# Kernel tuning notes

Measured on AMD Instinct MI355X. Metric: run time of the kernel, lower is better.

The kernel has to match this reference:

```python
import jax, jax.numpy as jnp
import numpy as np

B, L, F, H, DIM = 32, 1024, 1024, 1024, 1024


def setup_inputs() -> dict:
    key = jax.random.key(0)
    ks = jax.random.split(key, 8)
    features = jax.random.normal(ks[0], (B, L, F), dtype=jnp.float32)
    hidden = jax.random.normal(ks[1], (B, H), dtype=jnp.float32)
    # Dense layer params (glorot-ish scale)
    W1 = jax.random.normal(ks[2], (F, DIM), dtype=jnp.float32) / np.sqrt(F)
    b1 = jnp.zeros((DIM,), dtype=jnp.float32)
    W2 = jax.random.normal(ks[3], (H, DIM), dtype=jnp.float32) / np.sqrt(H)
    b2 = jnp.zeros((DIM,), dtype=jnp.float32)
    Wp = jax.random.normal(ks[4], (DIM, 1), dtype=jnp.float32) / np.sqrt(DIM)
    bp = jnp.zeros((1,), dtype=jnp.float32)
    return {"features": features, "hidden": hidden, "W1": W1, "b1": b1,
            "W2": W2, "b2": b2, "Wp": Wp, "bp": bp}


def reference(features, hidden, W1, b1, W2, b2, Wp, bp):
    # features: [B, L, F], hidden: [B, H]
    h1 = jnp.einsum('blf,fd->bld', features, W1) + b1          # [B, L, D]
    h2 = (hidden @ W2 + b2)[:, None, :]                         # [B, 1, D]
    att = jnp.tanh(h1 + h2)                                     # [B, L, D]
    score = jnp.einsum('bld,do->blo', att, Wp) + bp             # [B, L, 1]
    attention_weights = jax.nn.softmax(score, axis=1)           # [B, L, 1]
    context_vector = jnp.sum(attention_weights * features, axis=1)  # [B, F]
    return context_vector
```

## Files before the change

kernel.cpp:

```cpp
#include <hip/hip_runtime.h>
#include <hip/hip_bf16.h>


typedef __attribute__((ext_vector_type(8))) __bf16 bf16x8;
typedef __attribute__((ext_vector_type(4))) float f32x4;

static __device__ __forceinline__ ushort f2bf(float x) {
  unsigned u = __float_as_uint(x);
  return (ushort)((u + 0x7fffu + ((u >> 16) & 1u)) >> 16);
}

static __device__ __forceinline__ bf16x8 cvt8(float4 lo, float4 hi) {
  __hip_bfloat162 c0 = __float22bfloat162_rn({lo.x, lo.y});
  __hip_bfloat162 c1 = __float22bfloat162_rn({lo.z, lo.w});
  __hip_bfloat162 c2 = __float22bfloat162_rn({hi.x, hi.y});
  __hip_bfloat162 c3 = __float22bfloat162_rn({hi.z, hi.w});
  union { int4 i; bf16x8 v; } u;
  u.i.x = *(int*)&c0; u.i.y = *(int*)&c1; u.i.z = *(int*)&c2; u.i.w = *(int*)&c3;
  return u.v;
}

static __device__ __forceinline__ float tanh_fast(float x) {
  float e = __expf(2.f * x);
  return 1.f - 2.f / (e + 1.f);
}

__global__ __launch_bounds__(256) void prep_kernel(
    const float* __restrict__ W1, ushort* __restrict__ w1t,
    const float* __restrict__ hidden, const float* __restrict__ W2,
    const float* __restrict__ b2, float* __restrict__ h2p) {
  __shared__ float smem[64 * 65];
  const int bx = blockIdx.x, tid = threadIdx.x;
  if (bx < 256) {
    const int tc = bx & 15, tr = bx >> 4;
    float (*tt)[65] = (float(*)[65])smem;
    const int r = tid >> 4, c4 = (tid & 15) * 4;
#pragma unroll
    for (int p = 0; p < 4; ++p) {
      const int rr = p * 16 + r;
      float4 v = *(const float4*)(W1 + (size_t)(tr * 64 + rr) * 1024 + tc * 64 + c4);
      tt[rr][c4] = v.x; tt[rr][c4 + 1] = v.y; tt[rr][c4 + 2] = v.z; tt[rr][c4 + 3] = v.w;
    }
    __syncthreads();
    const int cc = tid >> 3, r8 = (tid & 7) * 8;
#pragma unroll
    for (int p = 0; p < 2; ++p) {
      const int c = p * 32 + cc;
      ushort tmp[8];
#pragma unroll
      for (int j = 0; j < 8; ++j) tmp[j] = f2bf(tt[r8 + j][c]);
      *(int4*)(w1t + (size_t)(tc * 64 + c) * 1024 + tr * 64 + r8) = *(int4*)tmp;
    }
  } else {
    const int t = bx - 256;
    const int dblk = t & 3, b = (t >> 2) & 31, z = t >> 7;
    const int d = dblk * 256 + tid;
    const int k0 = z * 128;
    float* h = smem;
    if (tid < 128) h[tid] = hidden[b * 1024 + k0 + tid];
    __syncthreads();
    float acc = (z == 0) ? b2[d] : 0.f;
#pragma unroll 8
    for (int k = 0; k < 128; ++k)
      acc += h[k] * W2[(size_t)(k0 + k) * 1024 + d];
    h2p[z * 32768 + b * 1024 + d] = acc;
  }
}


#define MFMA_ROW(AF, I)                                                        \
  acc[I][0] = __builtin_amdgcn_mfma_f32_16x16x32_bf16(AF, bf0, acc[I][0], 0, 0, 0); \
  acc[I][1] = __builtin_amdgcn_mfma_f32_16x16x32_bf16(AF, bf1, acc[I][1], 0, 0, 0); \
  acc[I][2] = __builtin_amdgcn_mfma_f32_16x16x32_bf16(AF, bf2, acc[I][2], 0, 0, 0); \
  acc[I][3] = __builtin_amdgcn_mfma_f32_16x16x32_bf16(AF, bf3, acc[I][3], 0, 0, 0);

#define TILE_STEP(T, CUR, NXT, AVIN, AVOUT) {                                  \
                                                      \
    bf16x8 bf0 = *(const bf16x8*)(bb + (T) * 32);                              \
    bf16x8 bf1 = *(const bf16x8*)(bb + 16384 + (T) * 32);                      \
    bf16x8 bf2 = *(const bf16x8*)(bb + 32768 + (T) * 32);                      \
    bf16x8 bf3 = *(const bf16x8*)(bb + 49152 + (T) * 32);                      \
                                                     \
    if ((T) + 2 < 32) {                                                        \
      const float* ap_ = feat + (size_t)(row0 + ar) * 1024 + ((T) + 2) * 32 + akof; \
      AVOUT[0] = *(const float4*)(ap_);                                        \
      AVOUT[1] = *(const float4*)(ap_ + 4);                                    \
      AVOUT[2] = *(const float4*)(ap_ + 8);                                    \
      AVOUT[3] = *(const float4*)(ap_ + 12);                                   \
    }                                                                          \
                                                    \
    bf16x8 af0 = *(const bf16x8*)&ldsA[CUR][wm * 64 + lrow][cswz8];            \
    bf16x8 af1 = *(const bf16x8*)&ldsA[CUR][wm * 64 + 16 + lrow][cswz8];       \
    bf16x8 af2 = *(const bf16x8*)&ldsA[CUR][wm * 64 + 32 + lrow][cswz8];       \
    bf16x8 af3 = *(const bf16x8*)&ldsA[CUR][wm * 64 + 48 + lrow][cswz8];       \
    MFMA_ROW(af0, 0); MFMA_ROW(af1, 1); MFMA_ROW(af2, 2); MFMA_ROW(af3, 3);    \
                                     \
    if ((T) + 1 < 32) {                                                        \
      union { bf16x8 v; int4 i; } w0_, w1_;                                    \
      w0_.v = cvt8(AVIN[0], AVIN[1]);                                          \
      w1_.v = cvt8(AVIN[2], AVIN[3]);                                          \
      *(int4*)&ldsA[NXT][ar][awz0] = w0_.i;                                    \
      *(int4*)&ldsA[NXT][ar][awz1] = w1_.i;                                    \
    }                                                                          \
    __syncthreads();                                                           \
  }

__global__ __launch_bounds__(256, 3) void gemm_score_kernel(
    const float* __restrict__ feat,
    const ushort* __restrict__ w1t,
    const float* __restrict__ b1, const float* __restrict__ h2p,
    const float* __restrict__ wp, float* __restrict__ score_p) {
  __shared__ ushort ldsA[2][128][32];
  __shared__ float sred[2][64];
  __shared__ float hbl[128], wpl[128];

  const int tid = threadIdx.x;
  const int row0 = blockIdx.x * 128;
  const int col0 = blockIdx.y * 128;
  const int b = blockIdx.x >> 3;

  const int wave = tid >> 6, lane = tid & 63;
  const int wm = wave & 1, wn = wave >> 1;
  const int lrow = lane & 15, quad = lane >> 4;
  const int cswz8 = (quad ^ ((lrow >> 1) & 3)) * 8;

  if (tid < 128) {
    const int d = col0 + tid;
    float hv = b1[d];
#pragma unroll
    for (int p = 0; p < 8; ++p) hv += h2p[p * 32768 + b * 1024 + d];
    hbl[tid] = hv;
  } else {
    wpl[tid - 128] = wp[col0 + tid - 128];
  }

  const int ar = tid >> 1;
  const int akof = (tid & 1) * 16;
  const int xr = (ar >> 1) & 3;
  const int awz0 = ((2 * (tid & 1) + 0) ^ xr) * 8;
  const int awz1 = ((2 * (tid & 1) + 1) ^ xr) * 8;

  const ushort* bb = w1t + (size_t)(col0 + wn * 64 + lrow) * 1024 + quad * 8;

  f32x4 acc[4][4] = {};
  float4 avA[4], avB[4];

  {
    const float* ap_ = feat + (size_t)(row0 + ar) * 1024 + akof;
    float4 v0 = *(const float4*)(ap_);
    float4 v1 = *(const float4*)(ap_ + 4);
    float4 v2 = *(const float4*)(ap_ + 8);
    float4 v3 = *(const float4*)(ap_ + 12);
    union { bf16x8 v; int4 i; } w0_, w1_;
    w0_.v = cvt8(v0, v1);
    w1_.v = cvt8(v2, v3);
    *(int4*)&ldsA[0][ar][awz0] = w0_.i;
    *(int4*)&ldsA[0][ar][awz1] = w1_.i;
    const float* ap1_ = ap_ + 32;
    avA[0] = *(const float4*)(ap1_);
    avA[1] = *(const float4*)(ap1_ + 4);
    avA[2] = *(const float4*)(ap1_ + 8);
    avA[3] = *(const float4*)(ap1_ + 12);
  }
  __syncthreads();

  for (int t = 0; t < 32; t += 2) {
    TILE_STEP(t, 0, 1, avA, avB);
    TILE_STEP(t + 1, 1, 0, avB, avA);
  }

  float hbv[4], wpv[4];
#pragma unroll
  for (int j = 0; j < 4; ++j) {
    const int idx = wn * 64 + j * 16 + lrow;
    hbv[j] = hbl[idx];
    wpv[j] = wpl[idx];
  }
  float rsum[4][4];
#pragma unroll
  for (int i = 0; i < 4; ++i) {
#pragma unroll
    for (int r = 0; r < 4; ++r) {
      float s = 0.f;
#pragma unroll
      for (int j = 0; j < 4; ++j)
        s += tanh_fast(acc[i][j][r] + hbv[j]) * wpv[j];
      s += __shfl_xor(s, 8);
      s += __shfl_xor(s, 4);
      s += __shfl_xor(s, 2);
      s += __shfl_xor(s, 1);
      rsum[i][r] = s;
    }
  }
  if (wn == 1 && lrow == 0) {
#pragma unroll
    for (int i = 0; i < 4; ++i)
#pragma unroll
      for (int r = 0; r < 4; ++r)
        sred[wm][i * 16 + quad * 4 + r] = rsum[i][r];
  }
  __syncthreads();
  if (wn == 0 && lrow == 0) {
#pragma unroll
    for (int i = 0; i < 4; ++i)
#pragma unroll
      for (int r = 0; r < 4; ++r) {
        const int ro = wm * 64 + i * 16 + quad * 4 + r;
        score_p[(size_t)blockIdx.y * 32768 + row0 + ro] =
            rsum[i][r] + sred[wm][ro & 63];
      }
  }
}

__global__ __launch_bounds__(256) void softmax_kernel(
    const float* __restrict__ score_p, float* __restrict__ w,
    float* __restrict__ out) {
  const int b = blockIdx.x, tid = threadIdx.x;
  const int lane = tid & 63, wv = tid >> 6;
  __shared__ float sm[4], ss[4];
  float v[4];
  float mx = -1e30f;
#pragma unroll
  for (int i = 0; i < 4; ++i) {
    const int idx = b * 1024 + i * 256 + tid;
    out[idx] = 0.f;
    float s = 0.f;
#pragma unroll
    for (int p = 0; p < 8; ++p) s += score_p[p * 32768 + idx];
    v[i] = s;
    mx = fmaxf(mx, s);
  }
#pragma unroll
  for (int off = 32; off; off >>= 1) mx = fmaxf(mx, __shfl_xor(mx, off));
  if (lane == 0) sm[wv] = mx;
  __syncthreads();
  mx = fmaxf(fmaxf(sm[0], sm[1]), fmaxf(sm[2], sm[3]));
  float sum = 0.f;
#pragma unroll
  for (int i = 0; i < 4; ++i) {
    v[i] = __expf(v[i] - mx);
    sum += v[i];
  }
#pragma unroll
  for (int off = 32; off; off >>= 1) sum += __shfl_xor(sum, off);
  if (lane == 0) ss[wv] = sum;
  __syncthreads();
  const float inv = 1.f / (ss[0] + ss[1] + ss[2] + ss[3]);
#pragma unroll
  for (int i = 0; i < 4; ++i) w[b * 1024 + i * 256 + tid] = v[i] * inv;
}

__global__ __launch_bounds__(256) void context_kernel(
    const float* __restrict__ w, const float* __restrict__ feat,
    float* __restrict__ out) {
  const int b = blockIdx.y;
  const int l0 = blockIdx.x * 64;
  const int f0 = threadIdx.x * 4;
  __shared__ float wl[64];
  if (threadIdx.x < 64) wl[threadIdx.x] = w[b * 1024 + l0 + threadIdx.x];
  __syncthreads();
  const float* fb = feat + (size_t)b * 1048576 + (size_t)l0 * 1024 + f0;
  float a0 = 0.f, a1 = 0.f, a2 = 0.f, a3 = 0.f;
#pragma unroll 8
  for (int l = 0; l < 64; ++l) {
    float4 v = *(const float4*)(fb + (size_t)l * 1024);
    const float wv = wl[l];
    a0 += wv * v.x;
    a1 += wv * v.y;
    a2 += wv * v.z;
    a3 += wv * v.w;
  }
  float* dst = out + b * 1024 + f0;
  atomicAdd(dst + 0, a0);
  atomicAdd(dst + 1, a1);
  atomicAdd(dst + 2, a2);
  atomicAdd(dst + 3, a3);
}

extern "C" void kernel_launch(void* const* d_in, const int* in_sizes, int n_in,
                              void* d_out, int out_size, void* d_ws, size_t ws_size,
                              hipStream_t stream) {
  const float* feat   = (const float*)d_in[0];
  const float* hidden = (const float*)d_in[1];
  const float* W1     = (const float*)d_in[2];
  const float* b1     = (const float*)d_in[3];
  const float* W2     = (const float*)d_in[4];
  const float* b2     = (const float*)d_in[5];
  const float* Wp     = (const float*)d_in[6];
  float* out = (float*)d_out;

  char* ws = (char*)d_ws;
  ushort* w1t    = (ushort*)ws;
  float* score_p = (float*)(ws + 2097152);
  float* h2p     = (float*)(ws + 3145728);
  float* wts     = (float*)(ws + 4194304);

  prep_kernel<<<1280, 256, 0, stream>>>(W1, w1t, hidden, W2, b2, h2p);
  gemm_score_kernel<<<dim3(256, 8), 256, 0, stream>>>(feat, w1t, b1, h2p, Wp,
                                                      score_p);
  softmax_kernel<<<32, 256, 0, stream>>>(score_p, wts, out);
  context_kernel<<<dim3(16, 32), 256, 0, stream>>>(wts, feat, out);
}
```

Before: 398.0 us.

## Make each GEMM block cover all columns so features are read once

The score GEMM is reorganised so each 512-thread block owns 64 rows and the full 1024 output columns, eight waves with 128 columns each. The fp32 features are then read and converted to bf16 only once instead of eight times across column blocks, and the partial-score buffer plus its reduction in softmax go away. B fragments are double-buffered in registers, with manual barriers and setprio around the MFMA burst. In exchange the tile is larger, which raises register pressure, the grid is smaller, and W1 is streamed by every block.

```diff
diff --git a/kernel.cpp b/kernel.cpp
--- a/kernel.cpp
+++ b/kernel.cpp
@@ -10,14 +10,13 @@
   return (ushort)((u + 0x7fffu + ((u >> 16) & 1u)) >> 16);
 }
 
-static __device__ __forceinline__ bf16x8 cvt8(float4 lo, float4 hi) {
-  __hip_bfloat162 c0 = __float22bfloat162_rn({lo.x, lo.y});
-  __hip_bfloat162 c1 = __float22bfloat162_rn({lo.z, lo.w});
-  __hip_bfloat162 c2 = __float22bfloat162_rn({hi.x, hi.y});
-  __hip_bfloat162 c3 = __float22bfloat162_rn({hi.z, hi.w});
-  union { int4 i; bf16x8 v; } u;
-  u.i.x = *(int*)&c0; u.i.y = *(int*)&c1; u.i.z = *(int*)&c2; u.i.w = *(int*)&c3;
-  return u.v;
+static __device__ __forceinline__ int2 cvt4(float4 v) {
+  __hip_bfloat162 c0 = __float22bfloat162_rn({v.x, v.y});
+  __hip_bfloat162 c1 = __float22bfloat162_rn({v.z, v.w});
+  int2 r;
+  r.x = *(int*)&c0;
+  r.y = *(int*)&c1;
+  return r;
 }
 
 static __device__ __forceinline__ float tanh_fast(float x) {
@@ -68,113 +67,99 @@
 }
 
 
-#define MFMA_ROW(AF, I)                                                        \
-  acc[I][0] = __builtin_amdgcn_mfma_f32_16x16x32_bf16(AF, bf0, acc[I][0], 0, 0, 0); \
-  acc[I][1] = __builtin_amdgcn_mfma_f32_16x16x32_bf16(AF, bf1, acc[I][1], 0, 0, 0); \
-  acc[I][2] = __builtin_amdgcn_mfma_f32_16x16x32_bf16(AF, bf2, acc[I][2], 0, 0, 0); \
-  acc[I][3] = __builtin_amdgcn_mfma_f32_16x16x32_bf16(AF, bf3, acc[I][3], 0, 0, 0);
-
-#define TILE_STEP(T, CUR, NXT, AVIN, AVOUT) {                                  \
-                                                      \
-    bf16x8 bf0 = *(const bf16x8*)(bb + (T) * 32);                              \
-    bf16x8 bf1 = *(const bf16x8*)(bb + 16384 + (T) * 32);                      \
-    bf16x8 bf2 = *(const bf16x8*)(bb + 32768 + (T) * 32);                      \
-    bf16x8 bf3 = *(const bf16x8*)(bb + 49152 + (T) * 32);                      \
-                                                     \
-    if ((T) + 2 < 32) {                                                        \
-      const float* ap_ = feat + (size_t)(row0 + ar) * 1024 + ((T) + 2) * 32 + akof; \
-      AVOUT[0] = *(const float4*)(ap_);                                        \
-      AVOUT[1] = *(const float4*)(ap_ + 4);                                    \
-      AVOUT[2] = *(const float4*)(ap_ + 8);                                    \
-      AVOUT[3] = *(const float4*)(ap_ + 12);                                   \
-    }                                                                          \
-                                                    \
-    bf16x8 af0 = *(const bf16x8*)&ldsA[CUR][wm * 64 + lrow][cswz8];            \
-    bf16x8 af1 = *(const bf16x8*)&ldsA[CUR][wm * 64 + 16 + lrow][cswz8];       \
-    bf16x8 af2 = *(const bf16x8*)&ldsA[CUR][wm * 64 + 32 + lrow][cswz8];       \
-    bf16x8 af3 = *(const bf16x8*)&ldsA[CUR][wm * 64 + 48 + lrow][cswz8];       \
-    MFMA_ROW(af0, 0); MFMA_ROW(af1, 1); MFMA_ROW(af2, 2); MFMA_ROW(af3, 3);    \
-                                     \
-    if ((T) + 1 < 32) {                                                        \
-      union { bf16x8 v; int4 i; } w0_, w1_;                                    \
-      w0_.v = cvt8(AVIN[0], AVIN[1]);                                          \
-      w1_.v = cvt8(AVIN[2], AVIN[3]);                                          \
-      *(int4*)&ldsA[NXT][ar][awz0] = w0_.i;                                    \
-      *(int4*)&ldsA[NXT][ar][awz1] = w1_.i;                                    \
-    }                                                                          \
-    __syncthreads();                                                           \
-  }
-
-__global__ __launch_bounds__(256, 3) void gemm_score_kernel(
+__global__ __launch_bounds__(512, 2) void gemm_score_kernel(
     const float* __restrict__ feat,
     const ushort* __restrict__ w1t,
     const float* __restrict__ b1, const float* __restrict__ h2p,
-    const float* __restrict__ wp, float* __restrict__ score_p) {
-  __shared__ ushort ldsA[2][128][32];
-  __shared__ float sred[2][64];
-  __shared__ float hbl[128], wpl[128];
+    const float* __restrict__ wp, float* __restrict__ score) {
+  __shared__ ushort ldsA[2][64][32];
+  __shared__ float hbl[1024], wpl[1024];
+  __shared__ float sred[7][64];
 
   const int tid = threadIdx.x;
-  const int row0 = blockIdx.x * 128;
-  const int col0 = blockIdx.y * 128;
-  const int b = blockIdx.x >> 3;
-
+  const int row0 = blockIdx.x * 64;
+  const int b = blockIdx.x >> 4;
   const int wave = tid >> 6, lane = tid & 63;
-  const int wm = wave & 1, wn = wave >> 1;
   const int lrow = lane & 15, quad = lane >> 4;
-  const int cswz8 = (quad ^ ((lrow >> 1) & 3)) * 8;
-
-  if (tid < 128) {
-    const int d = col0 + tid;
-    float hv = b1[d];
-#pragma unroll
-    for (int p = 0; p < 8; ++p) hv += h2p[p * 32768 + b * 1024 + d];
-    hbl[tid] = hv;
-  } else {
-    wpl[tid - 128] = wp[col0 + tid - 128];
-  }
-
-  const int ar = tid >> 1;
-  const int akof = (tid & 1) * 16;
-  const int xr = (ar >> 1) & 3;
-  const int awz0 = ((2 * (tid & 1) + 0) ^ xr) * 8;
-  const int awz1 = ((2 * (tid & 1) + 1) ^ xr) * 8;
-
-  const ushort* bb = w1t + (size_t)(col0 + wn * 64 + lrow) * 1024 + quad * 8;
-
-  f32x4 acc[4][4] = {};
-  float4 avA[4], avB[4];
 
   {
-    const float* ap_ = feat + (size_t)(row0 + ar) * 1024 + akof;
-    float4 v0 = *(const float4*)(ap_);
-    float4 v1 = *(const float4*)(ap_ + 4);
-    float4 v2 = *(const float4*)(ap_ + 8);
-    float4 v3 = *(const float4*)(ap_ + 12);
-    union { bf16x8 v; int4 i; } w0_, w1_;
-    w0_.v = cvt8(v0, v1);
-    w1_.v = cvt8(v2, v3);
-    *(int4*)&ldsA[0][ar][awz0] = w0_.i;
-    *(int4*)&ldsA[0][ar][awz1] = w1_.i;
-    const float* ap1_ = ap_ + 32;
-    avA[0] = *(const float4*)(ap1_);
-    avA[1] = *(const float4*)(ap1_ + 4);
-    avA[2] = *(const float4*)(ap1_ + 8);
-    avA[3] = *(const float4*)(ap1_ + 12);
-  }
-  __syncthreads();
-
-  for (int t = 0; t < 32; t += 2) {
-    TILE_STEP(t, 0, 1, avA, avB);
-    TILE_STEP(t + 1, 1, 0, avB, avA);
-  }
-
-  float hbv[4], wpv[4];
-#pragma unroll
-  for (int j = 0; j < 4; ++j) {
-    const int idx = wn * 64 + j * 16 + lrow;
-    hbv[j] = hbl[idx];
-    wpv[j] = wpl[idx];
+    const int d = tid * 2;
+    float2 hv = *(const float2*)(b1 + d);
+#pragma unroll
+    for (int p = 0; p < 8; ++p) {
+      float2 hp = *(const float2*)(h2p + p * 32768 + b * 1024 + d);
+      hv.x += hp.x;
+      hv.y += hp.y;
+    }
+    *(float2*)(hbl + d) = hv;
+    *(float2*)(wpl + d) = *(const float2*)(wp + d);
+  }
+
+  const int ar = tid >> 3;
+  const int asw = ((((tid & 7) >> 1) ^ ((ar >> 1) & 3)) * 8 + (tid & 1) * 4);
+  const float* aptr = feat + (size_t)(row0 + ar) * 1024 + (tid & 7) * 4;
+
+  const int acs = (quad ^ ((lrow >> 1) & 3)) * 8;
+
+  const ushort* bb[8];
+#pragma unroll
+  for (int j = 0; j < 8; ++j)
+    bb[j] = w1t + (size_t)(wave * 128 + j * 16 + lrow) * 1024 + quad * 8;
+
+  f32x4 acc[4][8] = {};
+  float4 avv[2];
+  bf16x8 bB[2][8];
+
+  {
+    float4 v0 = *(const float4*)(aptr);
+    *(int2*)&ldsA[0][ar][asw] = cvt4(v0);
+    avv[1] = *(const float4*)(aptr + 32);
+    avv[0] = *(const float4*)(aptr + 64);
+#pragma unroll
+    for (int j = 0; j < 8; ++j) bB[0][j] = *(const bf16x8*)(bb[j]);
+  }
+  asm volatile("s_waitcnt lgkmcnt(0)");
+  __builtin_amdgcn_sched_barrier(0);
+  __builtin_amdgcn_s_barrier();
+  __builtin_amdgcn_sched_barrier(0);
+
+#pragma unroll
+  for (int t = 0; t < 32; ++t) {
+    const int cur = t & 1, nxt = cur ^ 1;
+    bf16x8 af[4];
+#pragma unroll
+    for (int i = 0; i < 4; ++i)
+      af[i] = *(const bf16x8*)&ldsA[cur][i * 16 + lrow][acs];
+    if (t + 1 < 32) {
+#pragma unroll
+      for (int j = 0; j < 8; ++j)
+        bB[nxt][j] = *(const bf16x8*)(bb[j] + (t + 1) * 32);
+    }
+    if (t + 1 < 32)
+      *(int2*)&ldsA[nxt][ar][asw] = cvt4(avv[(t + 1) & 1]);
+    if (t + 3 < 32)
+      avv[(t + 1) & 1] = *(const float4*)(aptr + (t + 3) * 32);
+    __builtin_amdgcn_s_setprio(1);
+#pragma unroll
+    for (int i = 0; i < 4; ++i)
+#pragma unroll
+      for (int j = 0; j < 8; ++j)
+        acc[i][j] = __builtin_amdgcn_mfma_f32_16x16x32_bf16(
+            af[i], bB[cur][j], acc[i][j], 0, 0, 0);
+    __builtin_amdgcn_s_setprio(0);
+    __builtin_amdgcn_sched_barrier(0);
+    asm volatile("s_waitcnt lgkmcnt(0)");
+    __builtin_amdgcn_sched_barrier(0);
+    __builtin_amdgcn_s_barrier();
+    __builtin_amdgcn_sched_barrier(0);
+  }
+
+  float hbv[8], wpv[8];
+#pragma unroll
+  for (int j = 0; j < 8; ++j) {
+    const int c = wave * 128 + j * 16 + lrow;
+    hbv[j] = hbl[c];
+    wpv[j] = wpl[c];
   }
   float rsum[4][4];
 #pragma unroll
@@ -183,7 +168,7 @@
     for (int r = 0; r < 4; ++r) {
       float s = 0.f;
 #pragma unroll
-      for (int j = 0; j < 4; ++j)
+      for (int j = 0; j < 8; ++j)
         s += tanh_fast(acc[i][j][r] + hbv[j]) * wpv[j];
       s += __shfl_xor(s, 8);
       s += __shfl_xor(s, 4);
@@ -192,28 +177,30 @@
       rsum[i][r] = s;
     }
   }
-  if (wn == 1 && lrow == 0) {
+  if (wave != 0 && lrow == 0) {
 #pragma unroll
     for (int i = 0; i < 4; ++i)
 #pragma unroll
       for (int r = 0; r < 4; ++r)
-        sred[wm][i * 16 + quad * 4 + r] = rsum[i][r];
-  }
-  __syncthreads();
-  if (wn == 0 && lrow == 0) {
+        sred[wave - 1][i * 16 + quad * 4 + r] = rsum[i][r];
+  }
+  __syncthreads();
+  if (wave == 0 && lrow == 0) {
 #pragma unroll
     for (int i = 0; i < 4; ++i)
 #pragma unroll
       for (int r = 0; r < 4; ++r) {
-        const int ro = wm * 64 + i * 16 + quad * 4 + r;
-        score_p[(size_t)blockIdx.y * 32768 + row0 + ro] =
-            rsum[i][r] + sred[wm][ro & 63];
+        const int ro = i * 16 + quad * 4 + r;
+        float s = rsum[i][r];
+#pragma unroll
+        for (int w = 0; w < 7; ++w) s += sred[w][ro];
+        score[row0 + ro] = s;
       }
   }
 }
 
 __global__ __launch_bounds__(256) void softmax_kernel(
-    const float* __restrict__ score_p, float* __restrict__ w,
+    const float* __restrict__ score, float* __restrict__ w,
     float* __restrict__ out) {
   const int b = blockIdx.x, tid = threadIdx.x;
   const int lane = tid & 63, wv = tid >> 6;
@@ -224,11 +211,8 @@
   for (int i = 0; i < 4; ++i) {
     const int idx = b * 1024 + i * 256 + tid;
     out[idx] = 0.f;
-    float s = 0.f;
-#pragma unroll
-    for (int p = 0; p < 8; ++p) s += score_p[p * 32768 + idx];
-    v[i] = s;
-    mx = fmaxf(mx, s);
+    v[i] = score[idx];
+    mx = fmaxf(mx, v[i]);
   }
 #pragma unroll
   for (int off = 32; off; off >>= 1) mx = fmaxf(mx, __shfl_xor(mx, off));
@@ -290,14 +274,13 @@
   float* out = (float*)d_out;
 
   char* ws = (char*)d_ws;
-  ushort* w1t    = (ushort*)ws;
-  float* score_p = (float*)(ws + 2097152);
-  float* h2p     = (float*)(ws + 3145728);
-  float* wts     = (float*)(ws + 4194304);
+  ushort* w1t   = (ushort*)ws;
+  float* score  = (float*)(ws + 2097152);
+  float* h2p    = (float*)(ws + 3145728);
+  float* wts    = (float*)(ws + 4194304);
 
   prep_kernel<<<1280, 256, 0, stream>>>(W1, w1t, hidden, W2, b2, h2p);
-  gemm_score_kernel<<<dim3(256, 8), 256, 0, stream>>>(feat, w1t, b1, h2p, Wp,
-                                                      score_p);
-  softmax_kernel<<<32, 256, 0, stream>>>(score_p, wts, out);
+  gemm_score_kernel<<<512, 512, 0, stream>>>(feat, w1t, b1, h2p, Wp, score);
+  softmax_kernel<<<32, 256, 0, stream>>>(score, wts, out);
   context_kernel<<<dim3(16, 32), 256, 0, stream>>>(wts, feat, out);
 }
```

Result: faster. 358.7 us (-9.9%).
